# Kernel tuning notes

Measured on AMD Instinct MI355X. Metric: run time of the kernel, lower is better.

## Reference

```python
import jax, jax.numpy as jnp
import numpy as np
import math

B, IN_DIM, HID, OUT_DIM = 65536, 256, 512, 256
NUM_LAYERS = 3
ALPHA = 0.5
OSC_STRENGTH = 0.1


def _l2norm(v, eps=1e-12):
    return v / (jnp.linalg.norm(v) + eps)


def spectral_normalize(W, u):
    # One power-iteration step (torch spectral_norm forward, eval-style):
    # u, v are computed under no_grad; sigma = u^T W v is differentiable in W.
    v = jax.lax.stop_gradient(_l2norm(W.T @ u))
    u2 = jax.lax.stop_gradient(_l2norm(W @ v))
    sigma = jnp.dot(u2, W @ v)
    return W / sigma


def _osc_weight(dim, strength):
    # Block-diagonal 2x2 rotations (angle=0.1), scaled by oscillation_strength.
    W = np.zeros((dim, dim), dtype=np.float32)
    c, s = math.cos(0.1), math.sin(0.1)
    for i in range(0, dim - 1, 2):
        W[i, i] = c
        W[i, i + 1] = -s
        W[i + 1, i] = s
        W[i + 1, i + 1] = c
    return jnp.asarray(W * strength)


def setup_inputs() -> dict:
    key = jax.random.key(0)
    ks = jax.random.split(key, 10)
    lim_in = 1.0 / math.sqrt(IN_DIM)
    lim_h = 1.0 / math.sqrt(HID)
    return {
        "x": jax.random.normal(ks[0], (B, IN_DIM), dtype=jnp.float32),
        "W_in_w": jax.random.uniform(ks[1], (HID, IN_DIM), jnp.float32, -lim_in, lim_in),
        "W_in_b": jax.random.uniform(ks[2], (HID,), jnp.float32, -lim_in, lim_in),
        "layers_w": jax.random.uniform(ks[3], (NUM_LAYERS, HID, HID), jnp.float32, -lim_h, lim_h),
        "layers_b": jax.random.uniform(ks[4], (NUM_LAYERS, HID), jnp.float32, -lim_h, lim_h),
        "layers_u": jax.random.normal(ks[5], (NUM_LAYERS, HID), dtype=jnp.float32),
        "osc_w": _osc_weight(HID, OSC_STRENGTH),
        "osc_u": jax.random.normal(ks[6], (HID,), dtype=jnp.float32),
        "head_w": jax.random.uniform(ks[7], (OUT_DIM, HID), jnp.float32, -lim_h, lim_h),
        "head_b": jax.random.uniform(ks[8], (OUT_DIM,), jnp.float32, -lim_h, lim_h),
        "steps": 30,
    }


def reference(x, W_in_w, W_in_b, layers_w, layers_b, layers_u, osc_w, osc_u, head_w, head_b, steps):
    # Spectral-normalized weights are constant across integration steps.
    Wsn = jnp.stack([spectral_normalize(layers_w[l], layers_u[l]) for l in range(NUM_LAYERS)])  # [L,H,H]
    osc_sn = spectral_normalize(osc_w, osc_u)
    b_sum = layers_b.sum(axis=0)  # biases add linearly
    x_emb = x @ W_in_w.T + W_in_b  # [B,H], invariant across steps

    def step(_, h):
        t = jnp.tanh(h)
        # sum_l t @ Wsn[l]^T  (all layers see the same tanh(h))
        h_rec = x_emb + jnp.einsum("bh,lgh->bg", t, Wsn) + b_sum
        h_osc = h @ osc_sn.T
        h_target = jnp.tanh(h_rec + h_osc)
        return (1.0 - ALPHA) * h + ALPHA * h_target

    h0 = jnp.zeros((x.shape[0], HID), dtype=x.dtype)
    h = jax.lax.fori_loop(0, steps, step, h0)
    return h @ head_w.T + head_b
```

## Files before the change

kernel.cpp:

```cpp
#include <hip/hip_runtime.h>
#include <stdint.h>

#define HID 512
#define IND 256
#define OUTD 256
#define BROWS 32

typedef __attribute__((ext_vector_type(8))) short    short8;
typedef __attribute__((ext_vector_type(8))) _Float16 half8;
typedef __attribute__((ext_vector_type(4))) short    short4v;
typedef __attribute__((ext_vector_type(4))) float    f32x4;
typedef __attribute__((ext_vector_type(4))) int      i32x4;

#define MFMAH(a,b,c) __builtin_amdgcn_mfma_f32_16x16x32_f16(a,b,c,0,0,0)

__device__ __forceinline__ short f2bf(float f){
  uint32_t u = __builtin_bit_cast(uint32_t, f);
  u += 0x7FFFu + ((u>>16)&1u);
  return (short)(u>>16);
}
__device__ __forceinline__ float bf2f(short s){
  uint32_t u = ((uint32_t)(uint16_t)s) << 16;
  return __builtin_bit_cast(float, u);
}
__device__ __forceinline__ short f2h(float f){
  _Float16 h = (_Float16)f;
  return __builtin_bit_cast(short, h);
}
__device__ __forceinline__ float h2f(short s){
  return (float)__builtin_bit_cast(_Float16, s);
}
__device__ __forceinline__ int pack_hl(float v){
  short hi = f2bf(v);
  short lo = f2bf(v - bf2f(hi));
  return (((int)(uint16_t)hi) << 16) | (int)(uint16_t)lo;
}
__device__ __forceinline__ float unpk(int p){
  float vh = __builtin_bit_cast(float, (uint32_t)p & 0xFFFF0000u);
  float vl = __builtin_bit_cast(float, (uint32_t)p << 16);
  return vh + vl;
}
__device__ __forceinline__ float tanh_fast(float x){
  float e = __builtin_amdgcn_exp2f(x * 2.88539008177792681472f);
  return __builtin_fmaf(-2.0f, __builtin_amdgcn_rcpf(e + 1.0f), 1.0f);
}
__device__ __forceinline__ float neigh(float v){
  return __builtin_bit_cast(float,
      __builtin_amdgcn_mov_dpp(__builtin_bit_cast(int, v), 0xB1, 0xF, 0xF, true));
}
__device__ __forceinline__ uint32_t axor(uint32_t b){ return b ^ (((b>>7)&7u)<<4); }

__global__ void sigma_kernel(const float* __restrict__ lw, const float* __restrict__ lu,
                             const float* __restrict__ ow, const float* __restrict__ ou,
                             float* __restrict__ invs)
{
  __shared__ float sv[HID];
  __shared__ float red[8];
  const int g = threadIdx.x;
  const int m = blockIdx.x;
  const float* W = (m < 3) ? (lw + (size_t)m*HID*HID) : ow;
  const float* u = (m < 3) ? (lu + m*HID) : ou;
  float t1 = 0.f;
  for (int k = 0; k < HID; ++k) t1 += W[(size_t)k*HID + g] * u[k];
  float ss = t1*t1;
  #pragma unroll
  for (int d = 32; d; d >>= 1) ss += __shfl_xor(ss, d);
  if ((g & 63) == 0) red[g >> 6] = ss;
  __syncthreads();
  float tot = 0.f;
  #pragma unroll
  for (int i = 0; i < 8; ++i) tot += red[i];
  float nrm = sqrtf(tot);
  sv[g] = t1 / (nrm + 1e-12f);
  __syncthreads();
  float n = 0.f;
  const float* Wr = W + (size_t)g*HID;
  for (int k = 0; k < HID; ++k) n += Wr[k] * sv[k];
  float ss2 = n*n;
  #pragma unroll
  for (int d = 32; d; d >>= 1) ss2 += __shfl_xor(ss2, d);
  if ((g & 63) == 0) red[g >> 6] = ss2;
  __syncthreads();
  float tot2 = 0.f;
  #pragma unroll
  for (int i = 0; i < 8; ++i) tot2 += red[i];
  float nn = sqrtf(tot2);
  float sigma = tot2 / (nn + 1e-12f);
  if (g == 0) invs[m] = 1.0f / sigma;
}

__global__ void pack_wsum_f16(const float* __restrict__ lw, const float* __restrict__ invs,
                              short* __restrict__ pw)
{
  int i = blockIdx.x*blockDim.x + threadIdx.x;
  int j = i & 7, lane = (i >> 3) & 63, f = i >> 9;
  int kt = f >> 5, ctg = f & 31;
  int k = kt*32 + (lane >> 4)*8 + j;
  int g = ctg*16 + (lane & 15);
  size_t idx = (size_t)g*HID + k;
  float v = lw[idx]*invs[0] + lw[262144 + idx]*invs[1] + lw[524288 + idx]*invs[2];
  pw[i] = f2h(v);
}

template<int K, int N>
__global__ void pack_b_f16(const float* __restrict__ W, short* __restrict__ pb)
{
  int i = blockIdx.x*blockDim.x + threadIdx.x;
  int j = i & 7, lane = (i >> 3) & 63, f = i >> 9;
  constexpr int NCT = N/16;
  int kt = f / NCT, ctg = f % NCT;
  int k = kt*32 + (lane >> 4)*8 + j;
  int c = ctg*16 + (lane & 15);
  pb[i] = f2h(W[(size_t)c*K + k]);
}

__global__ void pack_small(const float* __restrict__ lb, const float* __restrict__ ow,
                           const float* __restrict__ invs,
                           float* __restrict__ bsum, float* __restrict__ cs, float* __restrict__ cn)
{
  int g = blockIdx.x*blockDim.x + threadIdx.x;
  if (g >= HID) return;
  bsum[g] = lb[g] + lb[HID + g] + lb[2*HID + g];
  float is = invs[3];
  cs[g] = ow[(size_t)g*HID + g] * is;
  cn[g] = ow[(size_t)g*HID + (g^1)] * is;
}

__global__ void __launch_bounds__(512) fused_main(
    const float* __restrict__ x,
    const float* __restrict__ winb,
    const float* __restrict__ headb,
    const int*  __restrict__ stepsp,
    const short* __restrict__ packW,
    const short* __restrict__ packI,
    const short* __restrict__ packHd,
    const float* __restrict__ bsumA,
    const float* __restrict__ csA,
    const float* __restrict__ cnA,
    float* __restrict__ out)
{
  __shared__ char ldsbuf[65536];
  char* ldsHi = ldsbuf;
  char* ldsLo = ldsbuf + 32768;
  const int tid  = threadIdx.x;
  const int lane = tid & 63;
  const int l15  = lane & 15;
  const int ql   = lane >> 4;
  const int wc   = tid >> 6;
  const int rb   = blockIdx.x;

  const uint32_t laneRd = (uint32_t)((lane*16) ^ (((lane>>3)&7)<<4));

  {
    const float* xb = x + (size_t)rb*BROWS*IND;
    #pragma unroll
    for (int i = 0; i < 4; ++i) {
      int fi  = i*512 + tid;
      int row = fi >> 6;
      int c   = (fi & 63)*4;
      f32x4 v = *(const f32x4*)(xb + (size_t)row*IND + c);
      short4v hi4, lo4;
      #pragma unroll
      for (int j = 0; j < 4; ++j) {
        short hh = f2h(v[j]);
        hi4[j] = hh;
        lo4[j] = f2h(v[j] - h2f(hh));
      }
      int rtg = row >> 4, kt = c >> 5, qd = (c >> 3) & 3;
      uint32_t byte = (uint32_t)(((rtg*8 + kt)*1024) + (qd*16 + (row & 15))*16 + (c & 7)*2);
      *(short4v*)(ldsHi + axor(byte)) = hi4;
      *(short4v*)(ldsLo + axor(byte)) = lo4;
    }
  }
  __syncthreads();

  const int nsteps = stepsp[0];

  const float cs_s = csA[wc*64 + l15];
  const float cn_s = cnA[wc*64 + l15];

  f32x4 h[2][4];
  i32x4 xp[2][4];
  {
    f32x4 acc[2][4];
    #pragma unroll
    for (int ct = 0; ct < 4; ++ct) {
      int c = wc*64 + ct*16 + l15;
      float s = winb[c] + bsumA[c];
      #pragma unroll
      for (int rt = 0; rt < 2; ++rt) {
        f32x4 z; z[0]=s; z[1]=s; z[2]=s; z[3]=s;
        acc[rt][ct] = z;
      }
    }
    {
      const char* pI = (const char*)packI + (size_t)wc*4096 + (size_t)lane*16;
      __builtin_amdgcn_s_setprio(1);
      #pragma unroll 2
      for (int kt = 0; kt < 8; ++kt) {
        half8 b0 = *(const half8*)(pI);
        half8 b1 = *(const half8*)(pI + 1024);
        half8 b2 = *(const half8*)(pI + 2048);
        half8 b3 = *(const half8*)(pI + 3072);
        #pragma unroll
        for (int rt = 0; rt < 2; ++rt) {
          half8 ah = *(const half8*)(ldsHi + laneRd + (rt*8 + kt)*1024);
          half8 al = *(const half8*)(ldsLo + laneRd + (rt*8 + kt)*1024);
          acc[rt][0] = MFMAH(ah, b0, acc[rt][0]);
          acc[rt][0] = MFMAH(al, b0, acc[rt][0]);
          acc[rt][1] = MFMAH(ah, b1, acc[rt][1]);
          acc[rt][1] = MFMAH(al, b1, acc[rt][1]);
          acc[rt][2] = MFMAH(ah, b2, acc[rt][2]);
          acc[rt][2] = MFMAH(al, b2, acc[rt][2]);
          acc[rt][3] = MFMAH(ah, b3, acc[rt][3]);
          acc[rt][3] = MFMAH(al, b3, acc[rt][3]);
        }
        pI += 32768;
      }
      __builtin_amdgcn_s_setprio(0);
    }
    #pragma unroll
    for (int rt = 0; rt < 2; ++rt)
      #pragma unroll
      for (int ct = 0; ct < 4; ++ct)
        #pragma unroll
        for (int r = 0; r < 4; ++r) {
          float xv = acc[rt][ct][r];
          xp[rt][ct][r] = pack_hl(xv);
          h[rt][ct][r] = (nsteps >= 1) ? 0.5f * tanh_fast(xv) : 0.f;
        }
  }
  __syncthreads();

  const char* baseW = (const char*)packW + (size_t)wc*4096 + (size_t)lane*16;

  for (int s = 1; s < nsteps; ++s) {
    #pragma unroll
    for (int rt = 0; rt < 2; ++rt) {
      uint32_t rcomp = (uint32_t)(rt*16384);
      #pragma unroll
      for (int ct = 0; ct < 4; ++ct) {
        int c = wc*64 + ct*16 + l15;
        uint32_t wcomp = (uint32_t)(((c >> 5)*1024) + (((c >> 3) & 3)*256) + ((c & 7)*2) + ql*64);
        #pragma unroll
        for (int r = 0; r < 4; ++r) {
          float t = tanh_fast(h[rt][ct][r]);
          uint32_t byte = axor(rcomp + wcomp + (uint32_t)(r*16));
          *(short*)(ldsHi + byte) = f2h(t);
        }
      }
    }
    __syncthreads();

    f32x4 acc[2][4];
    #pragma unroll
    for (int rt = 0; rt < 2; ++rt)
      #pragma unroll
      for (int ct = 0; ct < 4; ++ct)
        #pragma unroll
        for (int r = 0; r < 4; ++r) {
          float hv = h[rt][ct][r];
          acc[rt][ct][r] = __builtin_fmaf(cs_s, hv,
                             __builtin_fmaf(cn_s, neigh(hv), unpk(xp[rt][ct][r])));
        }
    {
      const char* p = baseW;
      __builtin_amdgcn_s_setprio(1);
      #pragma unroll 4
      for (int kt = 0; kt < 16; ++kt) {
        half8 b0 = *(const half8*)(p);
        half8 b1 = *(const half8*)(p + 1024);
        half8 b2 = *(const half8*)(p + 2048);
        half8 b3 = *(const half8*)(p + 3072);
        #pragma unroll
        for (int rt = 0; rt < 2; ++rt) {
          half8 ah = *(const half8*)(ldsHi + laneRd + (rt*16 + kt)*1024);
          acc[rt][0] = MFMAH(ah, b0, acc[rt][0]);
          acc[rt][1] = MFMAH(ah, b1, acc[rt][1]);
          acc[rt][2] = MFMAH(ah, b2, acc[rt][2]);
          acc[rt][3] = MFMAH(ah, b3, acc[rt][3]);
        }
        p += 32768;
      }
      __builtin_amdgcn_s_setprio(0);
    }
    #pragma unroll
    for (int rt = 0; rt < 2; ++rt)
      #pragma unroll
      for (int ct = 0; ct < 4; ++ct)
        #pragma unroll
        for (int r = 0; r < 4; ++r)
          h[rt][ct][r] = __builtin_fmaf(0.5f, tanh_fast(acc[rt][ct][r]), 0.5f*h[rt][ct][r]);
    __syncthreads();
  }

  #pragma unroll
  for (int rt = 0; rt < 2; ++rt) {
    uint32_t rcomp = (uint32_t)(rt*16384);
    #pragma unroll
    for (int ct = 0; ct < 4; ++ct) {
      int c = wc*64 + ct*16 + l15;
      uint32_t wcomp = (uint32_t)(((c >> 5)*1024) + (((c >> 3) & 3)*256) + ((c & 7)*2) + ql*64);
      #pragma unroll
      for (int r = 0; r < 4; ++r) {
        float hv = h[rt][ct][r];
        short hh = f2h(hv);
        uint32_t byte = axor(rcomp + wcomp + (uint32_t)(r*16));
        *(short*)(ldsHi + byte) = hh;
        *(short*)(ldsLo + byte) = f2h(hv - h2f(hh));
      }
    }
  }
  __syncthreads();

  int oc[2]; float hbv[2];
  #pragma unroll
  for (int c2 = 0; c2 < 2; ++c2) { oc[c2] = wc*32 + c2*16 + l15; hbv[c2] = headb[oc[c2]]; }
  f32x4 o[2][2];
  #pragma unroll
  for (int rt = 0; rt < 2; ++rt)
    #pragma unroll
    for (int c2 = 0; c2 < 2; ++c2) {
      f32x4 z; z[0]=hbv[c2]; z[1]=hbv[c2]; z[2]=hbv[c2]; z[3]=hbv[c2];
      o[rt][c2] = z;
    }
  {
    const char* pHd = (const char*)packHd + (size_t)wc*2048 + (size_t)lane*16;
    #pragma unroll 2
    for (int kt = 0; kt < 16; ++kt) {
      #pragma unroll
      for (int rt = 0; rt < 2; ++rt) {
        half8 ah = *(const half8*)(ldsHi + laneRd + (rt*16 + kt)*1024);
        half8 al = *(const half8*)(ldsLo + laneRd + (rt*16 + kt)*1024);
        #pragma unroll
        for (int c2 = 0; c2 < 2; ++c2) {
          half8 b = *(const half8*)(pHd + c2*1024);
          o[rt][c2] = MFMAH(ah, b, o[rt][c2]);
          o[rt][c2] = MFMAH(al, b, o[rt][c2]);
        }
      }
      pHd += 16384;
    }
  }
  const size_t rowg = (size_t)rb*BROWS;
  #pragma unroll
  for (int rt = 0; rt < 2; ++rt)
    #pragma unroll
    for (int c2 = 0; c2 < 2; ++c2)
      #pragma unroll
      for (int r = 0; r < 4; ++r) {
        size_t row = rowg + rt*16 + ql*4 + r;
        out[row*OUTD + oc[c2]] = o[rt][c2][r];
      }
}

extern "C" void kernel_launch(void* const* d_in, const int* in_sizes, int n_in,
                              void* d_out, int out_size, void* d_ws, size_t ws_size,
                              hipStream_t stream)
{
  const float* x    = (const float*)d_in[0];
  const float* winw = (const float*)d_in[1];
  const float* winb = (const float*)d_in[2];
  const float* lw   = (const float*)d_in[3];
  const float* lb   = (const float*)d_in[4];
  const float* lu   = (const float*)d_in[5];
  const float* ow   = (const float*)d_in[6];
  const float* ou   = (const float*)d_in[7];
  const float* hw   = (const float*)d_in[8];
  const float* hb   = (const float*)d_in[9];
  const int*   st   = (const int*)d_in[10];
  float* out = (float*)d_out;
  char*  ws  = (char*)d_ws;

  float* invs   = (float*)(ws);
  float* bsum   = (float*)(ws + 1024);
  float* cs     = (float*)(ws + 4096);
  float* cn     = (float*)(ws + 8192);
  short* packW  = (short*)(ws + 16384);
  short* packI  = (short*)(ws + 16384 + 524288);
  short* packHd = (short*)(ws + 16384 + 524288 + 262144);

  sigma_kernel<<<4, 512, 0, stream>>>(lw, lu, ow, ou, invs);
  pack_wsum_f16<<<1024, 256, 0, stream>>>(lw, invs, packW);
  pack_b_f16<256, 512><<<512, 256, 0, stream>>>(winw, packI);
  pack_b_f16<512, 256><<<512, 256, 0, stream>>>(hw, packHd);
  pack_small<<<2, 256, 0, stream>>>(lb, ow, invs, bsum, cs, cn);

  fused_main<<<65536/BROWS, 512, 0, stream>>>(x, winb, hb, st,
                                              packW, packI, packHd,
                                              bsum, cs, cn, out);
}
```

Before: 1.577 ms.

## Double rows per block to 64 and keep x embedding in AGPRs

Each block now handles 64 batch rows instead of 32, doubling LDS to 128KB, so each weight fragment loaded from global/L2 is reused across four row tiles per step. The precomputed input embedding is stored as full fp32 in accumulator registers instead of a packed bf16 hi/lo pair, which frees VGPRs and removes the unpack arithmetic. The initial input projection is split into two column halves to limit register pressure. This halves the grid size and raises per-thread register use, which may reduce occupancy and latency hiding.

```diff
diff --git a/kernel.cpp b/kernel.cpp
--- a/kernel.cpp
+++ b/kernel.cpp
@@ -4,25 +4,15 @@
 #define HID 512
 #define IND 256
 #define OUTD 256
-#define BROWS 32
+#define BROWS 64
 
 typedef __attribute__((ext_vector_type(8))) short    short8;
 typedef __attribute__((ext_vector_type(8))) _Float16 half8;
 typedef __attribute__((ext_vector_type(4))) short    short4v;
 typedef __attribute__((ext_vector_type(4))) float    f32x4;
-typedef __attribute__((ext_vector_type(4))) int      i32x4;
 
 #define MFMAH(a,b,c) __builtin_amdgcn_mfma_f32_16x16x32_f16(a,b,c,0,0,0)
 
-__device__ __forceinline__ short f2bf(float f){
-  uint32_t u = __builtin_bit_cast(uint32_t, f);
-  u += 0x7FFFu + ((u>>16)&1u);
-  return (short)(u>>16);
-}
-__device__ __forceinline__ float bf2f(short s){
-  uint32_t u = ((uint32_t)(uint16_t)s) << 16;
-  return __builtin_bit_cast(float, u);
-}
 __device__ __forceinline__ short f2h(float f){
   _Float16 h = (_Float16)f;
   return __builtin_bit_cast(short, h);
@@ -30,15 +20,15 @@
 __device__ __forceinline__ float h2f(short s){
   return (float)__builtin_bit_cast(_Float16, s);
 }
-__device__ __forceinline__ int pack_hl(float v){
-  short hi = f2bf(v);
-  short lo = f2bf(v - bf2f(hi));
-  return (((int)(uint16_t)hi) << 16) | (int)(uint16_t)lo;
-}
-__device__ __forceinline__ float unpk(int p){
-  float vh = __builtin_bit_cast(float, (uint32_t)p & 0xFFFF0000u);
-  float vl = __builtin_bit_cast(float, (uint32_t)p << 16);
-  return vh + vl;
+__device__ __forceinline__ int to_agpr(int v){
+  int a;
+  asm("v_accvgpr_write_b32 %0, %1" : "=a"(a) : "v"(v));
+  return a;
+}
+__device__ __forceinline__ int from_agpr(int a){
+  int v;
+  asm("v_accvgpr_read_b32 %0, %1" : "=v"(v) : "a"(a));
+  return v;
 }
 __device__ __forceinline__ float tanh_fast(float x){
   float e = __builtin_amdgcn_exp2f(x * 2.88539008177792681472f);
@@ -139,9 +129,9 @@
     const float* __restrict__ cnA,
     float* __restrict__ out)
 {
-  __shared__ char ldsbuf[65536];
+  __shared__ char ldsbuf[131072];
   char* ldsHi = ldsbuf;
-  char* ldsLo = ldsbuf + 32768;
+  char* ldsLo = ldsbuf + 65536;
   const int tid  = threadIdx.x;
   const int lane = tid & 63;
   const int l15  = lane & 15;
@@ -154,7 +144,7 @@
   {
     const float* xb = x + (size_t)rb*BROWS*IND;
     #pragma unroll
-    for (int i = 0; i < 4; ++i) {
+    for (int i = 0; i < 8; ++i) {
       int fi  = i*512 + tid;
       int row = fi >> 6;
       int c   = (fi & 63)*4;
@@ -179,56 +169,53 @@
   const float cs_s = csA[wc*64 + l15];
   const float cn_s = cnA[wc*64 + l15];
 
-  f32x4 h[2][4];
-  i32x4 xp[2][4];
-  {
-    f32x4 acc[2][4];
-    #pragma unroll
-    for (int ct = 0; ct < 4; ++ct) {
-      int c = wc*64 + ct*16 + l15;
+  f32x4 h[4][4];
+  int xpa[4][4][4];
+  #pragma unroll
+  for (int ch = 0; ch < 2; ++ch) {
+    f32x4 acc[4][2];
+    #pragma unroll
+    for (int c2 = 0; c2 < 2; ++c2) {
+      int c = wc*64 + (ch*2 + c2)*16 + l15;
       float s = winb[c] + bsumA[c];
       #pragma unroll
-      for (int rt = 0; rt < 2; ++rt) {
+      for (int rt = 0; rt < 4; ++rt) {
         f32x4 z; z[0]=s; z[1]=s; z[2]=s; z[3]=s;
-        acc[rt][ct] = z;
+        acc[rt][c2] = z;
       }
     }
     {
-      const char* pI = (const char*)packI + (size_t)wc*4096 + (size_t)lane*16;
+      const char* pI = (const char*)packI + (size_t)wc*4096 + (size_t)(ch*2048) + (size_t)lane*16;
       __builtin_amdgcn_s_setprio(1);
       #pragma unroll 2
       for (int kt = 0; kt < 8; ++kt) {
         half8 b0 = *(const half8*)(pI);
         half8 b1 = *(const half8*)(pI + 1024);
-        half8 b2 = *(const half8*)(pI + 2048);
-        half8 b3 = *(const half8*)(pI + 3072);
-        #pragma unroll
-        for (int rt = 0; rt < 2; ++rt) {
+        #pragma unroll
+        for (int rt = 0; rt < 4; ++rt) {
           half8 ah = *(const half8*)(ldsHi + laneRd + (rt*8 + kt)*1024);
           half8 al = *(const half8*)(ldsLo + laneRd + (rt*8 + kt)*1024);
           acc[rt][0] = MFMAH(ah, b0, acc[rt][0]);
           acc[rt][0] = MFMAH(al, b0, acc[rt][0]);
           acc[rt][1] = MFMAH(ah, b1, acc[rt][1]);
           acc[rt][1] = MFMAH(al, b1, acc[rt][1]);
-          acc[rt][2] = MFMAH(ah, b2, acc[rt][2]);
-          acc[rt][2] = MFMAH(al, b2, acc[rt][2]);
-          acc[rt][3] = MFMAH(ah, b3, acc[rt][3]);
-          acc[rt][3] = MFMAH(al, b3, acc[rt][3]);
         }
         pI += 32768;
       }
       __builtin_amdgcn_s_setprio(0);
     }
     #pragma unroll
-    for (int rt = 0; rt < 2; ++rt)
-      #pragma unroll
-      for (int ct = 0; ct < 4; ++ct)
+    for (int rt = 0; rt < 4; ++rt)
+      #pragma unroll
+      for (int c2 = 0; c2 < 2; ++c2) {
+        int ct = ch*2 + c2;
         #pragma unroll
         for (int r = 0; r < 4; ++r) {
-          float xv = acc[rt][ct][r];
-          xp[rt][ct][r] = pack_hl(xv);
+          float xv = acc[rt][c2][r];
+          xpa[rt][ct][r] = to_agpr(__builtin_bit_cast(int, xv));
           h[rt][ct][r] = (nsteps >= 1) ? 0.5f * tanh_fast(xv) : 0.f;
         }
+      }
   }
   __syncthreads();
 
@@ -236,7 +223,7 @@
 
   for (int s = 1; s < nsteps; ++s) {
     #pragma unroll
-    for (int rt = 0; rt < 2; ++rt) {
+    for (int rt = 0; rt < 4; ++rt) {
       uint32_t rcomp = (uint32_t)(rt*16384);
       #pragma unroll
       for (int ct = 0; ct < 4; ++ct) {
@@ -252,28 +239,29 @@
     }
     __syncthreads();
 
-    f32x4 acc[2][4];
-    #pragma unroll
-    for (int rt = 0; rt < 2; ++rt)
+    f32x4 acc[4][4];
+    #pragma unroll
+    for (int rt = 0; rt < 4; ++rt)
       #pragma unroll
       for (int ct = 0; ct < 4; ++ct)
         #pragma unroll
         for (int r = 0; r < 4; ++r) {
           float hv = h[rt][ct][r];
+          float xe = __builtin_bit_cast(float, from_agpr(xpa[rt][ct][r]));
           acc[rt][ct][r] = __builtin_fmaf(cs_s, hv,
-                             __builtin_fmaf(cn_s, neigh(hv), unpk(xp[rt][ct][r])));
+                             __builtin_fmaf(cn_s, neigh(hv), xe));
         }
     {
       const char* p = baseW;
       __builtin_amdgcn_s_setprio(1);
-      #pragma unroll 4
+      #pragma unroll 2
       for (int kt = 0; kt < 16; ++kt) {
         half8 b0 = *(const half8*)(p);
         half8 b1 = *(const half8*)(p + 1024);
         half8 b2 = *(const half8*)(p + 2048);
         half8 b3 = *(const half8*)(p + 3072);
         #pragma unroll
-        for (int rt = 0; rt < 2; ++rt) {
+        for (int rt = 0; rt < 4; ++rt) {
           half8 ah = *(const half8*)(ldsHi + laneRd + (rt*16 + kt)*1024);
           acc[rt][0] = MFMAH(ah, b0, acc[rt][0]);
           acc[rt][1] = MFMAH(ah, b1, acc[rt][1]);
@@ -285,7 +273,7 @@
       __builtin_amdgcn_s_setprio(0);
     }
     #pragma unroll
-    for (int rt = 0; rt < 2; ++rt)
+    for (int rt = 0; rt < 4; ++rt)
       #pragma unroll
       for (int ct = 0; ct < 4; ++ct)
         #pragma unroll
@@ -295,7 +283,7 @@
   }
 
   #pragma unroll
-  for (int rt = 0; rt < 2; ++rt) {
+  for (int rt = 0; rt < 4; ++rt) {
     uint32_t rcomp = (uint32_t)(rt*16384);
     #pragma unroll
     for (int ct = 0; ct < 4; ++ct) {
@@ -316,9 +304,9 @@
   int oc[2]; float hbv[2];
   #pragma unroll
   for (int c2 = 0; c2 < 2; ++c2) { oc[c2] = wc*32 + c2*16 + l15; hbv[c2] = headb[oc[c2]]; }
-  f32x4 o[2][2];
-  #pragma unroll
-  for (int rt = 0; rt < 2; ++rt)
+  f32x4 o[4][2];
+  #pragma unroll
+  for (int rt = 0; rt < 4; ++rt)
     #pragma unroll
     for (int c2 = 0; c2 < 2; ++c2) {
       f32x4 z; z[0]=hbv[c2]; z[1]=hbv[c2]; z[2]=hbv[c2]; z[3]=hbv[c2];
@@ -329,7 +317,7 @@
     #pragma unroll 2
     for (int kt = 0; kt < 16; ++kt) {
       #pragma unroll
-      for (int rt = 0; rt < 2; ++rt) {
+      for (int rt = 0; rt < 4; ++rt) {
         half8 ah = *(const half8*)(ldsHi + laneRd + (rt*16 + kt)*1024);
         half8 al = *(const half8*)(ldsLo + laneRd + (rt*16 + kt)*1024);
         #pragma unroll
@@ -344,7 +332,7 @@
   }
   const size_t rowg = (size_t)rb*BROWS;
   #pragma unroll
-  for (int rt = 0; rt < 2; ++rt)
+  for (int rt = 0; rt < 4; ++rt)
     #pragma unroll
     for (int c2 = 0; c2 < 2; ++c2)
       #pragma unroll
```

After: 5.247 ms. +232.7%, slower.
